# Kernel tuning notes

Measured on AMD Instinct MI355X. Metric: run time of the kernel, lower is better.

The kernel has to match this reference:

```python
import jax, jax.numpy as jnp
import numpy as np


def _unfold3x3(x):
    # Matches torch F.unfold(kernel=(3,3), padding=1): output (B, C*9, H*W)
    # with feature layout (c, kh, kw) -- channel-major, kernel-position minor.
    B, C, H, W = x.shape
    xp = jnp.pad(x, ((0, 0), (0, 0), (1, 1), (1, 1)))
    patches = jnp.stack(
        [xp[:, :, i:i + H, j:j + W] for i in range(3) for j in range(3)],
        axis=2,
    )  # (B, C, 9, H, W)
    return patches.reshape(B, C * 9, H * W)


def setup_inputs() -> dict:
    key = jax.random.key(0)
    x = jax.random.normal(key, (4, 64, 64, 64), dtype=jnp.float32)
    return {"x": x}


def reference(x):
    B, C, H, W = x.shape
    HW = H * W
    xu = _unfold3x3(x)  # (B, C*9, HW)
    # torch F.normalize(dim=2): L2-normalize each (b, feature) row over spatial dim
    norm = jnp.maximum(jnp.linalg.norm(xu, axis=2, keepdims=True), 1e-12)
    xu = xu / norm
    # dense correlation over all positions: (B, HW, HW)
    R = jnp.einsum('bdn,bdm->bnm', xu, xu)
    _, idx = jax.lax.top_k(R, 3)  # idx: (B, HW, 3)
    # gather the top-3 neighbor patch columns; fixed k=3 loop (structural, not data dim)
    stacks = []
    for k in range(3):
        idx_k = idx[:, :, k][:, None, :]                    # (B, 1, HW)
        g = jnp.take_along_axis(xu, idx_k, axis=2)          # (B, C*9, HW)
        # torch: permute(0,2,1).reshape(B, HW, -1, C) -> (B, HW, 9, C)
        stacks.append(jnp.transpose(g, (0, 2, 1)).reshape(B, HW, 9, C))
    K = jnp.concatenate(stacks, axis=2)                     # (B, HW, 27, C)
    Q = jnp.transpose(x.reshape(B, C, HW), (0, 2, 1))       # (B, HW, C)
    scores = jnp.einsum('bnc,bnkc->bnk', Q, K) / jnp.sqrt(jnp.float32(C))
    w = jax.nn.softmax(scores, axis=2)                      # (B, HW, 27)
    return jnp.einsum('bnk,bnkc->bnc', w, K)                # (B, HW, C)
```

## Files before the change

kernel.cpp:

```cpp
#include <hip/hip_runtime.h>
#include <cstdint>

typedef short short8 __attribute__((ext_vector_type(8)));
typedef float f32x16 __attribute__((ext_vector_type(16)));

#define NB 4
#define NN 4096
#define ND 576
#define BIGI 0x7FFFFFFF
#define NSLICE 16

#define INVN_OFF 9437184
#define CANDV_OFF 9439488
#define CANDI_OFF 10225920

#define MFMA __builtin_amdgcn_mfma_f32_32x32x16_bf16

__device__ __forceinline__ unsigned short f2bf(float f) {
    unsigned u = __float_as_uint(f);
    u += 0x7FFFu + ((u >> 16) & 1u);
    return (unsigned short)(u >> 16);
}

__device__ __forceinline__ void insert_cmp(float v, int m,
    float& v0, int& i0, float& v1, int& i1, float& v2, int& i2) {
    bool beat2 = (v > v2) || (v == v2 && m < i2);
    if (beat2) {
        bool beat1 = (v > v1) || (v == v1 && m < i1);
        if (beat1) {
            v2 = v1; i2 = i1;
            bool beat0 = (v > v0) || (v == v0 && m < i0);
            if (beat0) { v1 = v0; i1 = i0; v0 = v; i0 = m; }
            else       { v1 = v;  i1 = m; }
        } else { v2 = v; i2 = m; }
    }
}

__global__ __launch_bounds__(64) void norm_kernel(const float* __restrict__ x,
                                                  float* __restrict__ ws) {
    const int bc = blockIdx.x;
    const int lane = threadIdx.x;
    const float* xp = x + ((size_t)bc << 12);
    float colsum = 0.f, v0 = 0.f, v63 = 0.f;
    for (int h = 0; h < 64; ++h) {
        const float val = xp[(h << 6) + lane];
        const float sq = val * val;
        colsum += sq;
        if (h == 0)  v0 = sq;
        if (h == 63) v63 = sq;
    }
    float total = colsum, row0 = v0, row63 = v63;
    #pragma unroll
    for (int o = 32; o > 0; o >>= 1) {
        total += __shfl_xor(total, o);
        row0  += __shfl_xor(row0, o);
        row63 += __shfl_xor(row63, o);
    }
    const float col0  = __shfl(colsum, 0);
    const float col63 = __shfl(colsum, 63);
    const float c00 = __shfl(v0, 0),  c0e = __shfl(v0, 63);
    const float ce0 = __shfl(v63, 0), cee = __shfl(v63, 63);
    if (lane < 9) {
        const int dh = lane / 3 - 1, dw = lane % 3 - 1;
        float S = total;
        if (dh == 1)  S -= row0;
        if (dh == -1) S -= row63;
        if (dw == 1)  S -= col0;
        if (dw == -1) S -= col63;
        if (dh == 1  && dw == 1)  S += c00;
        if (dh == 1  && dw == -1) S += c0e;
        if (dh == -1 && dw == 1)  S += ce0;
        if (dh == -1 && dw == -1) S += cee;
        float nrm = fmaxf(sqrtf(S), 1e-12f);
        ws[INVN_OFF + bc * 9 + lane] = 1.0f / nrm;
    }
}

__global__ __launch_bounds__(256) void mat_kernel(const float* __restrict__ x,
                                                  float* __restrict__ ws) {
    const int bi = blockIdx.x;
    const int b = bi / 576;
    const int rem = bi - b * 576;
    const int nt = rem / 18;
    const int kc = rem - nt * 18;
    unsigned short* AH = (unsigned short*)ws;
    unsigned short* AL = AH + 9437184;
    const float* invn = ws + INVN_OFF + b * 576;
    const int tid = threadIdx.x;
    #pragma unroll
    for (int hf2 = 0; hf2 < 2; ++hf2) {
        const int g = tid + hf2 * 256;
        const int row = g >> 2, cp = g & 3;
        const int c = cp ^ ((row >> 1) & 3);
        const int k0 = c * 8;
        const int n = nt * 128 + row;
        const int h = n >> 6, wc = n & 63;
        union { unsigned short us[8]; float4 f4; } uh, ul;
        #pragma unroll
        for (int j = 0; j < 8; ++j) {
            const int d = kc * 32 + k0 + j;
            const int ch = d / 9;
            const int p = d - ch * 9;
            const int r = h + p / 3 - 1, s2 = wc + p % 3 - 1;
            float val = 0.f;
            if ((unsigned)r < 64u && (unsigned)s2 < 64u)
                val = x[((size_t)(b * 64 + ch) << 12) + (r << 6) + s2];
            val *= invn[d];
            const unsigned short hb = f2bf(val);
            const float hfv = __uint_as_float(((unsigned)hb) << 16);
            const unsigned short lb = f2bf(val - hfv);
            uh.us[j] = hb; ul.us[j] = lb;
        }
        ((float4*)AH)[(size_t)bi * 512 + g] = uh.f4;
        ((float4*)AL)[(size_t)bi * 512 + g] = ul.f4;
    }
}

__device__ __forceinline__ short8 ldfragG(const unsigned short* p) {
    union { short8 s8; float4 f4; } u;
    u.f4 = *(const float4*)p;
    return u.s8;
}

__global__ void __launch_bounds__(256, 2) gram_kernel(float* ws) {
    __shared__ float cv[1536];
    __shared__ int   ci[1536];
    const int bx = blockIdx.x;
    const int r = bx >> 8;
    const int t = bx & 255;
    const int x = t & 7, g = t >> 3;
    const int b = r >> 1;
    const int half = r & 1;
    const int nt = 16 * half + 4 * (x >> 1) + (g >> 3);
    const int ms = 8 * (x & 1) + (g & 7);
    const int tid = threadIdx.x;
    const int w = tid >> 6, lane = tid & 63;
    const int l31 = lane & 31, kh2 = lane >> 5;

    const unsigned short* AH = (const unsigned short*)ws;
    const unsigned short* AL = AH + 9437184;

    const unsigned short* gAn[2] = {
        AH + (size_t)((b * 32 + nt) * 18) * 4096,
        AL + (size_t)((b * 32 + nt) * 18) * 4096 };
    const unsigned short* gAm[2][2];
    #pragma unroll
    for (int mi = 0; mi < 2; ++mi) {
        const int tile = 2 * ms + ((2 * w + mi) >> 2);
        gAm[mi][0] = AH + (size_t)((b * 32 + tile) * 18) * 4096;
        gAm[mi][1] = AL + (size_t)((b * 32 + tile) * 18) * 4096;
    }

    int boff[4][2], aoff[2][2];
    #pragma unroll
    for (int ni = 0; ni < 4; ++ni)
        #pragma unroll
        for (int h = 0; h < 2; ++h) {
            const int row = ni * 32 + l31;
            const int c = kh2 + 2 * h;
            boff[ni][h] = row * 32 + (c ^ ((row >> 1) & 3)) * 8;
        }
    #pragma unroll
    for (int mi = 0; mi < 2; ++mi)
        #pragma unroll
        for (int h = 0; h < 2; ++h) {
            const int row = (w * 64 + mi * 32 + l31) & 127;
            const int c = kh2 + 2 * h;
            aoff[mi][h] = row * 32 + (c ^ ((row >> 1) & 3)) * 8;
        }

    f32x16 acc[2][4];
    #pragma unroll
    for (int mi = 0; mi < 2; ++mi)
        #pragma unroll
        for (int ni = 0; ni < 4; ++ni)
            #pragma unroll
            for (int e = 0; e < 16; ++e) acc[mi][ni][e] = 0.f;

    for (int kc = 0; kc < 18; ++kc) {
        const int kb = kc * 4096;
        #pragma unroll
        for (int h = 0; h < 2; ++h) {
            short8 amh[2], aml[2], bh[4], bl[4];
            #pragma unroll
            for (int mi = 0; mi < 2; ++mi) {
                amh[mi] = ldfragG(gAm[mi][0] + kb + aoff[mi][h]);
                aml[mi] = ldfragG(gAm[mi][1] + kb + aoff[mi][h]);
            }
            #pragma unroll
            for (int ni = 0; ni < 4; ++ni) {
                bh[ni] = ldfragG(gAn[0] + kb + boff[ni][h]);
                bl[ni] = ldfragG(gAn[1] + kb + boff[ni][h]);
            }
            #pragma unroll
            for (int ni = 0; ni < 4; ++ni)
                #pragma unroll
                for (int mi = 0; mi < 2; ++mi) {
                    acc[mi][ni] = MFMA(amh[mi], bh[ni], acc[mi][ni], 0, 0, 0);
                    acc[mi][ni] = MFMA(amh[mi], bl[ni], acc[mi][ni], 0, 0, 0);
                    acc[mi][ni] = MFMA(aml[mi], bh[ni], acc[mi][ni], 0, 0, 0);
                }
        }
    }

    float t0v[4], t1v[4], t2v[4];
    int   t0i[4], t1i[4], t2i[4];
    #pragma unroll
    for (int i = 0; i < 4; ++i) {
        t0v[i] = t1v[i] = t2v[i] = -INFINITY;
        t0i[i] = t1i[i] = t2i[i] = BIGI;
    }
    const int mbase = ms * 256 + w * 64 + kh2 * 4;
    #pragma unroll
    for (int ni = 0; ni < 4; ++ni)
        #pragma unroll
        for (int mi = 0; mi < 2; ++mi)
            #pragma unroll
            for (int v = 0; v < 16; ++v) {
                const int m = mbase + mi * 32 + (v & 3) + 8 * (v >> 2);
                insert_cmp(acc[mi][ni][v], m,
                           t0v[ni], t0i[ni], t1v[ni], t1i[ni], t2v[ni], t2i[ni]);
            }

    #pragma unroll
    for (int ni = 0; ni < 4; ++ni) {
        const float pv0 = __shfl_xor(t0v[ni], 32);
        const float pv1 = __shfl_xor(t1v[ni], 32);
        const float pv2 = __shfl_xor(t2v[ni], 32);
        const int pi0 = __shfl_xor(t0i[ni], 32);
        const int pi1 = __shfl_xor(t1i[ni], 32);
        const int pi2 = __shfl_xor(t2i[ni], 32);
        insert_cmp(pv0, pi0, t0v[ni], t0i[ni], t1v[ni], t1i[ni], t2v[ni], t2i[ni]);
        insert_cmp(pv1, pi1, t0v[ni], t0i[ni], t1v[ni], t1i[ni], t2v[ni], t2i[ni]);
        insert_cmp(pv2, pi2, t0v[ni], t0i[ni], t1v[ni], t1i[ni], t2v[ni], t2i[ni]);
    }
    __syncthreads();
    if (kh2 == 0) {
        #pragma unroll
        for (int ni = 0; ni < 4; ++ni) {
            const int base2 = ((w * 4 + ni) * 32 + l31) * 3;
            cv[base2] = t0v[ni]; cv[base2 + 1] = t1v[ni]; cv[base2 + 2] = t2v[ni];
            ci[base2] = t0i[ni]; ci[base2 + 1] = t1i[ni]; ci[base2 + 2] = t2i[ni];
        }
    }
    __syncthreads();
    if (tid < 128) {
        const int ni = tid >> 5, l = tid & 31;
        float v0 = -INFINITY, v1 = -INFINITY, v2 = -INFINITY;
        int i0 = BIGI, i1 = BIGI, i2 = BIGI;
        #pragma unroll
        for (int w2 = 0; w2 < 4; ++w2) {
            const int base2 = ((w2 * 4 + ni) * 32 + l) * 3;
            #pragma unroll
            for (int j = 0; j < 3; ++j)
                insert_cmp(cv[base2 + j], ci[base2 + j], v0, i0, v1, i1, v2, i2);
        }
        const int n_glob = nt * 128 + ni * 32 + l;
        const size_t o = ((size_t)(b * NSLICE + ms) * NN + n_glob) * 3;
        ws[CANDV_OFF + o] = v0; ws[CANDV_OFF + o + 1] = v1; ws[CANDV_OFF + o + 2] = v2;
        unsigned short* wi = (unsigned short*)(ws + CANDI_OFF);
        wi[o] = (unsigned short)i0; wi[o + 1] = (unsigned short)i1; wi[o + 2] = (unsigned short)i2;
    }
}

__global__ __launch_bounds__(256) void attn_kernel(const float* __restrict__ x,
                                                   const float* __restrict__ ws,
                                                   float* __restrict__ out) {
    const int wid = threadIdx.x >> 6;
    const int lane = threadIdx.x & 63;
    const int gw = blockIdx.x * 4 + wid;
    const int b = gw >> 12;
    const int n = gw & 4095;

    float v0 = -INFINITY, v1 = -INFINITY, v2 = -INFINITY;
    int i0 = BIGI, i1 = BIGI, i2 = BIGI;
    const unsigned short* wi = (const unsigned short*)(ws + CANDI_OFF);
    for (int s = 0; s < NSLICE; ++s) {
        const size_t o = ((size_t)(b * NSLICE + s) * NN + n) * 3;
        #pragma unroll
        for (int j = 0; j < 3; ++j)
            insert_cmp(ws[CANDV_OFF + o + j], (int)wi[o + j], v0, i0, v1, i1, v2, i2);
    }
    const int idx3[3] = {i0, i1, i2};

    int cc[9], dhh[9], dww[9];
    float inr[9];
    #pragma unroll
    for (int a = 0; a < 9; ++a) {
        const int d = a * 64 + lane;
        const int c = d / 9;
        const int p = d - c * 9;
        cc[a] = c; dhh[a] = p / 3 - 1; dww[a] = p - (p / 3) * 3 - 1;
        inr[a] = ws[INVN_OFF + b * ND + d];
    }
    const float q = x[((size_t)(b * 64 + lane) << 12) + n];

    float rv[27], sc[27];
    #pragma unroll
    for (int k = 0; k < 3; ++k) {
        const int m = idx3[k];
        const int hm = m >> 6, wm = m & 63;
        #pragma unroll
        for (int a = 0; a < 9; ++a) {
            const int r = hm + dhh[a], s2 = wm + dww[a];
            float val = 0.f;
            if ((unsigned)r < 64u && (unsigned)s2 < 64u)
                val = x[((size_t)(b * 64 + cc[a]) << 12) + (r << 6) + s2];
            const float rr = val * inr[a];
            rv[k * 9 + a] = rr;
            float t = q * rr;
            #pragma unroll
            for (int o2 = 32; o2 > 0; o2 >>= 1) t += __shfl_xor(t, o2);
            sc[k * 9 + a] = t * 0.125f;
        }
    }
    float mx = -INFINITY;
    #pragma unroll
    for (int u = 0; u < 27; ++u) mx = fmaxf(mx, sc[u]);
    float sum = 0.f;
    #pragma unroll
    for (int u = 0; u < 27; ++u) { const float e = expf(sc[u] - mx); sc[u] = e; sum += e; }
    const float inv = 1.0f / sum;
    float o = 0.f;
    #pragma unroll
    for (int u = 0; u < 27; ++u) o += sc[u] * rv[u];
    out[((size_t)gw << 6) + lane] = o * inv;
}

extern "C" void kernel_launch(void* const* d_in, const int* in_sizes, int n_in,
                              void* d_out, int out_size, void* d_ws, size_t ws_size,
                              hipStream_t stream) {
    (void)in_sizes; (void)n_in; (void)out_size; (void)ws_size;
    const float* x = (const float*)d_in[0];
    float* ws = (float*)d_ws;
    float* out = (float*)d_out;

    hipLaunchKernelGGL(norm_kernel, dim3(NB * 64), dim3(64), 0, stream, x, ws);
    hipLaunchKernelGGL(mat_kernel, dim3(2304), dim3(256), 0, stream, x, ws);
    hipLaunchKernelGGL(gram_kernel, dim3(2048), dim3(256), 0, stream, ws);
    hipLaunchKernelGGL(attn_kernel, dim3(4096), dim3(256), 0, stream, x, ws, out);
}
```

Before: 808.3 us.

## Store matrix in MFMA fragment order and double-buffer gram kernel global loads

The matrix-building kernel now writes each 128x32 bf16 tile in the exact per-lane fragment order the MFMA consumes, so every lane of a wave reads a contiguous 16-byte chunk at lane*8. The gram kernel drops the XOR-swizzled offset tables and uses simple strided addresses. It also software-pipelines the K loop with two register fragment sets, loading the next half-chunk while the current one feeds MFMAs, to hide global load latency. The extra fragment set raises register pressure, which could hurt occupancy under launch_bounds(256,2).

```diff
diff --git a/kernel.cpp b/kernel.cpp
--- a/kernel.cpp
+++ b/kernel.cpp
@@ -90,9 +90,11 @@
     #pragma unroll
     for (int hf2 = 0; hf2 < 2; ++hf2) {
         const int g = tid + hf2 * 256;
-        const int row = g >> 2, cp = g & 3;
-        const int c = cp ^ ((row >> 1) & 3);
-        const int k0 = c * 8;
+        const int lane6 = g & 63;
+        const int hcl = (g >> 6) & 1;
+        const int sub = g >> 7;
+        const int row = sub * 32 + (lane6 & 31);
+        const int k0 = hcl * 16 + (lane6 >> 5) * 8;
         const int n = nt * 128 + row;
         const int h = n >> 6, wc = n & 63;
         union { unsigned short us[8]; float4 f4; } uh, ul;
@@ -140,34 +142,18 @@
     const unsigned short* AH = (const unsigned short*)ws;
     const unsigned short* AL = AH + 9437184;
 
-    const unsigned short* gAn[2] = {
-        AH + (size_t)((b * 32 + nt) * 18) * 4096,
-        AL + (size_t)((b * 32 + nt) * 18) * 4096 };
+    const unsigned short* gAn[2];
+    gAn[0] = AH + (size_t)((b * 32 + nt) * 18) * 4096 + lane * 8;
+    gAn[1] = AL + (size_t)((b * 32 + nt) * 18) * 4096 + lane * 8;
     const unsigned short* gAm[2][2];
+    int subm[2];
     #pragma unroll
     for (int mi = 0; mi < 2; ++mi) {
         const int tile = 2 * ms + ((2 * w + mi) >> 2);
-        gAm[mi][0] = AH + (size_t)((b * 32 + tile) * 18) * 4096;
-        gAm[mi][1] = AL + (size_t)((b * 32 + tile) * 18) * 4096;
-    }
-
-    int boff[4][2], aoff[2][2];
-    #pragma unroll
-    for (int ni = 0; ni < 4; ++ni)
-        #pragma unroll
-        for (int h = 0; h < 2; ++h) {
-            const int row = ni * 32 + l31;
-            const int c = kh2 + 2 * h;
-            boff[ni][h] = row * 32 + (c ^ ((row >> 1) & 3)) * 8;
-        }
-    #pragma unroll
-    for (int mi = 0; mi < 2; ++mi)
-        #pragma unroll
-        for (int h = 0; h < 2; ++h) {
-            const int row = (w * 64 + mi * 32 + l31) & 127;
-            const int c = kh2 + 2 * h;
-            aoff[mi][h] = row * 32 + (c ^ ((row >> 1) & 3)) * 8;
-        }
+        subm[mi] = (2 * w + mi) & 3;
+        gAm[mi][0] = AH + (size_t)((b * 32 + tile) * 18) * 4096 + lane * 8;
+        gAm[mi][1] = AL + (size_t)((b * 32 + tile) * 18) * 4096 + lane * 8;
+    }
 
     f32x16 acc[2][4];
     #pragma unroll
@@ -177,31 +163,44 @@
             #pragma unroll
             for (int e = 0; e < 16; ++e) acc[mi][ni][e] = 0.f;
 
+    short8 P0[12], P1[12];
+
+    #define LOADSET(P, kc, h)                                                   \
+        {                                                                       \
+            const int kb_ = (kc) * 4096;                                        \
+            _Pragma("unroll")                                                   \
+            for (int ni = 0; ni < 4; ++ni) {                                    \
+                P[ni]     = ldfragG(gAn[0] + kb_ + (ni * 2 + (h)) * 512);       \
+                P[4 + ni] = ldfragG(gAn[1] + kb_ + (ni * 2 + (h)) * 512);       \
+            }                                                                   \
+            _Pragma("unroll")                                                   \
+            for (int mi = 0; mi < 2; ++mi) {                                    \
+                P[8 + mi]  = ldfragG(gAm[mi][0] + kb_ + (subm[mi] * 2 + (h)) * 512); \
+                P[10 + mi] = ldfragG(gAm[mi][1] + kb_ + (subm[mi] * 2 + (h)) * 512); \
+            }                                                                   \
+        }
+
+    #define COMPUTESET(P)                                                       \
+        {                                                                       \
+            _Pragma("unroll")                                                   \
+            for (int ni = 0; ni < 4; ++ni)                                      \
+                _Pragma("unroll")                                               \
+                for (int mi = 0; mi < 2; ++mi) {                                \
+                    acc[mi][ni] = MFMA(P[8 + mi],  P[ni],     acc[mi][ni], 0, 0, 0); \
+                    acc[mi][ni] = MFMA(P[8 + mi],  P[4 + ni], acc[mi][ni], 0, 0, 0); \
+                    acc[mi][ni] = MFMA(P[10 + mi], P[ni],     acc[mi][ni], 0, 0, 0); \
+                }                                                               \
+        }
+
+    LOADSET(P0, 0, 0);
     for (int kc = 0; kc < 18; ++kc) {
-        const int kb = kc * 4096;
-        #pragma unroll
-        for (int h = 0; h < 2; ++h) {
-            short8 amh[2], aml[2], bh[4], bl[4];
-            #pragma unroll
-            for (int mi = 0; mi < 2; ++mi) {
-                amh[mi] = ldfragG(gAm[mi][0] + kb + aoff[mi][h]);
-                aml[mi] = ldfragG(gAm[mi][1] + kb + aoff[mi][h]);
-            }
-            #pragma unroll
-            for (int ni = 0; ni < 4; ++ni) {
-                bh[ni] = ldfragG(gAn[0] + kb + boff[ni][h]);
-                bl[ni] = ldfragG(gAn[1] + kb + boff[ni][h]);
-            }
-            #pragma unroll
-            for (int ni = 0; ni < 4; ++ni)
-                #pragma unroll
-                for (int mi = 0; mi < 2; ++mi) {
-                    acc[mi][ni] = MFMA(amh[mi], bh[ni], acc[mi][ni], 0, 0, 0);
-                    acc[mi][ni] = MFMA(amh[mi], bl[ni], acc[mi][ni], 0, 0, 0);
-                    acc[mi][ni] = MFMA(aml[mi], bh[ni], acc[mi][ni], 0, 0, 0);
-                }
-        }
-    }
+        LOADSET(P1, kc, 1);
+        COMPUTESET(P0);
+        if (kc < 17) LOADSET(P0, kc + 1, 0);
+        COMPUTESET(P1);
+    }
+    #undef LOADSET
+    #undef COMPUTESET
 
     float t0v[4], t1v[4], t2v[4];
     int   t0i[4], t1i[4], t2i[4];
```

After: 777.7 us. 1.04x faster.
